# Kernel optimization log

Hardware: AMD Instinct MI355X
Metric: run time of the kernel (lower is better)

Reference implementation:

```python
import jax, jax.numpy as jnp
import numpy as np

N_NODES = 50000
N_EDGES = 800000
D_IN = 128
D_OUT = 128


def setup_inputs() -> dict:
    key = jax.random.key(0)
    k1, k2, k3, k4, k5, k6 = jax.random.split(key, 6)
    stdv = 1.0 / np.sqrt(D_OUT)
    x = jax.random.normal(k1, (N_NODES, D_IN), dtype=jnp.float32)
    weight = jax.random.uniform(k2, (D_IN, D_OUT), dtype=jnp.float32, minval=-stdv, maxval=stdv)
    bias = jax.random.uniform(k3, (D_OUT,), dtype=jnp.float32, minval=-stdv, maxval=stdv)
    edge_weight = jax.random.uniform(k4, (N_EDGES,), dtype=jnp.float32)
    edge_row = jax.random.randint(k5, (N_EDGES,), 0, N_NODES, dtype=jnp.int64)
    edge_col = jax.random.randint(k6, (N_EDGES,), 0, N_NODES, dtype=jnp.int64)
    return {"x": x, "weight": weight, "bias": bias,
            "edge_weight": edge_weight, "edge_row": edge_row, "edge_col": edge_col}


def reference(x, weight, bias, edge_weight, edge_row, edge_col):
    # support = input @ W   -> [N, D_OUT]
    support = x @ weight
    # spmm(adj, support): out[i] = sum over edges (i<-j) of a_ij * support[j]
    gathered = support[edge_col] * edge_weight[:, None]  # [E, D_OUT]
    out = jax.ops.segment_sum(gathered, edge_row, num_segments=N_NODES)
    return out + bias
```

## Files before the change

kernel.cpp:

```cpp
#include <hip/hip_runtime.h>
#include <hip/hip_bf16.h>

#define NN 50000
#define NE 800000
#define D 128

#define RPB 50
#define NB 1000
#define NBP 1024
#define CAP 1024
#define TILE 4096
#define NBIN 196
#define AROWS 64
#define TSTR 136

#define CASTB 1563
#define PACKB 4

#define XH_OFF   0
#define WF_OFF   3200000
#define CUR_OFF  3208192
#define REC_OFF  3209216

typedef short bf16x8 __attribute__((ext_vector_type(8)));
typedef float f32x4 __attribute__((ext_vector_type(4)));

__device__ inline unsigned short f2bf_u(float f) {
    __hip_bfloat16 h = __float2bfloat16(f);
    return __builtin_bit_cast(unsigned short, h);
}
__device__ inline unsigned pack2(float a, float b) {
    return (unsigned)f2bf_u(a) | ((unsigned)f2bf_u(b) << 16);
}
__device__ inline void acc8(float* acc, uint4 v, float w) {
    unsigned dw[4] = {v.x, v.y, v.z, v.w};
    #pragma unroll
    for (int i = 0; i < 4; ++i) {
        float lo = __int_as_float((int)(dw[i] << 16));
        float hi = __int_as_float((int)(dw[i] & 0xffff0000u));
        acc[2 * i]     += w * lo;
        acc[2 * i + 1] += w * hi;
    }
}

__global__ __launch_bounds__(512) void cast_bin_kernel(
    const float* __restrict__ x, const float* __restrict__ W,
    const int* __restrict__ erow, const int* __restrict__ ecol,
    const float* __restrict__ ew,
    unsigned* __restrict__ x_h4, unsigned short* __restrict__ Wf,
    int* __restrict__ cursor, int2* __restrict__ recs)
{
    __shared__ int  lhist[NBP];
    __shared__ int  lexcl[NBP];
    __shared__ int  lbase[NBP];
    __shared__ int  lpair[512];
    __shared__ int2 stag[TILE];

    int b = blockIdx.x;
    int t = threadIdx.x;

    if (b < CASTB) {
        int idx = b * 512 + t;
        if (idx < 800000) {
            const float4* x4 = (const float4*)x;
            float4 v0 = x4[idx * 2];
            float4 v1 = x4[idx * 2 + 1];
            uint4 o;
            o.x = pack2(v0.x, v0.y);
            o.y = pack2(v0.z, v0.w);
            o.z = pack2(v1.x, v1.y);
            o.w = pack2(v1.z, v1.w);
            ((uint4*)x_h4)[idx] = o;
        }
        return;
    }
    if (b < CASTB + PACKB) {
        int flat = (b - CASTB) * 512 + t;
        int lane = flat & 63;
        int c    = (flat >> 6) & 3;
        int nt   = flat >> 8;
        int col  = nt * 16 + (lane & 15);
        int kb   = c * 32 + (lane >> 4) * 8;
        unsigned d[4];
        #pragma unroll
        for (int jj = 0; jj < 4; ++jj) {
            float a  = W[(kb + 2 * jj) * D + col];
            float bb = W[(kb + 2 * jj + 1) * D + col];
            d[jj] = pack2(a, bb);
        }
        uint4 o; o.x = d[0]; o.y = d[1]; o.z = d[2]; o.w = d[3];
        ((uint4*)Wf)[flat] = o;
        return;
    }

    int base = (b - CASTB - PACKB) * TILE;
    int cnt = NE - base; if (cnt > TILE) cnt = TILE;

    lhist[t] = 0;
    lhist[t + 512] = 0;
    __syncthreads();

    int4 r[2], c[2]; float4 w[2]; bool val[2];
    #pragma unroll
    for (int g = 0; g < 2; ++g) {
        int i4 = (base >> 2) + t + g * 512;
        val[g] = (i4 * 4) < NE && (i4 * 4) < (base + TILE);
        if (val[g]) {
            r[g] = ((const int4*)erow)[i4];
            c[g] = ((const int4*)ecol)[i4];
            w[g] = ((const float4*)ew)[i4];
        }
    }
    #pragma unroll
    for (int g = 0; g < 2; ++g) {
        if (val[g]) {
            atomicAdd(&lhist[(unsigned)r[g].x / RPB], 1);
            atomicAdd(&lhist[(unsigned)r[g].y / RPB], 1);
            atomicAdd(&lhist[(unsigned)r[g].z / RPB], 1);
            atomicAdd(&lhist[(unsigned)r[g].w / RPB], 1);
        }
    }
    __syncthreads();

    int a0 = lhist[2 * t], a1 = lhist[2 * t + 1];
    lpair[t] = a0 + a1;
    __syncthreads();
    for (int off = 1; off < 512; off <<= 1) {
        int v = (t >= off) ? lpair[t - off] : 0;
        __syncthreads();
        lpair[t] += v;
        __syncthreads();
    }
    int exclp = lpair[t] - (a0 + a1);
    lexcl[2 * t]     = exclp;
    lexcl[2 * t + 1] = exclp + a0;
    lbase[2 * t]     = a0 ? atomicAdd(&cursor[2 * t], a0) : 0;
    lbase[2 * t + 1] = a1 ? atomicAdd(&cursor[2 * t + 1], a1) : 0;
    lhist[2 * t]     = exclp;
    lhist[2 * t + 1] = exclp + a0;
    __syncthreads();

    #pragma unroll
    for (int g = 0; g < 2; ++g) {
        if (val[g]) {
            int rr[4] = {r[g].x, r[g].y, r[g].z, r[g].w};
            int cc[4] = {c[g].x, c[g].y, c[g].z, c[g].w};
            float wwv[4] = {w[g].x, w[g].y, w[g].z, w[g].w};
            #pragma unroll
            for (int j = 0; j < 4; ++j) {
                int bk = (unsigned)rr[j] / RPB;
                int rank = atomicAdd(&lhist[bk], 1);
                int2 rec;
                rec.x = (rr[j] << 16) | cc[j];
                rec.y = __float_as_int(wwv[j]);
                stag[rank] = rec;
            }
        }
    }
    __syncthreads();

    #pragma unroll
    for (int k = 0; k < 8; ++k) {
        int i = t + k * 512;
        if (i < cnt) {
            int2 rec = stag[i];
            int bk = (((unsigned)rec.x) >> 16) / RPB;
            int pos = lbase[bk] + (i - lexcl[bk]);
            if (pos < CAP)
                recs[(size_t)bk * CAP + pos] = rec;
        }
    }
}

__global__ __launch_bounds__(512) void gat_gemm_kernel(
    const unsigned short* __restrict__ x_h, const int2* __restrict__ recs,
    const int* __restrict__ cursor, const unsigned short* __restrict__ Wf,
    const float* __restrict__ bias, float* __restrict__ out)
{
    __shared__ int2 srec[CAP];
    __shared__ __align__(16) unsigned short tile[AROWS * TSTR];
    __shared__ int rowstart[RPB + 1];
    __shared__ int rowcur[64];
    __shared__ int stmp[64];

    int t = threadIdx.x;
    int b = blockIdx.x;
    int cnt = cursor[b];
    if (cnt > CAP) cnt = CAP;
    int rb = b * RPB;
    const int2* my = recs + (size_t)b * CAP;

    if (t < 64) rowcur[t] = 0;
    __syncthreads();

    int2 r0, r1;
    bool v0 = t < cnt, v1 = t + 512 < cnt;
    if (v0) r0 = my[t];
    if (v1) r1 = my[t + 512];

    if (v0) atomicAdd(&rowcur[(((unsigned)r0.x) >> 16) - rb], 1);
    if (v1) atomicAdd(&rowcur[(((unsigned)r1.x) >> 16) - rb], 1);
    __syncthreads();

    int myc = 0;
    if (t < 64) { myc = rowcur[t]; stmp[t] = myc; }
    __syncthreads();
    for (int off = 1; off < 64; off <<= 1) {
        int v = 0;
        if (t < 64 && t >= off) v = stmp[t - off];
        __syncthreads();
        if (t < 64) stmp[t] += v;
        __syncthreads();
    }
    if (t < 64) { int ex = stmp[t] - myc; if (t <= RPB) rowstart[t] = ex; rowcur[t] = ex; }
    if (t == 0) rowstart[RPB] = cnt;
    __syncthreads();

    if (v0) srec[atomicAdd(&rowcur[(((unsigned)r0.x) >> 16) - rb], 1)] = r0;
    if (v1) srec[atomicAdd(&rowcur[(((unsigned)r1.x) >> 16) - rb], 1)] = r1;
    __syncthreads();

    int q = t & 15;
    int grp = t >> 4;
    const uint4* xv = (const uint4*)x_h;
    #pragma unroll
    for (int it = 0; it < 2; ++it) {
        int rl = it * 32 + grp;
        if (rl < RPB) {
            int p = rowstart[rl], p1 = rowstart[rl + 1];
            float acc[8] = {};
            for (; p + 4 <= p1; p += 4) {
                int2 e0 = srec[p];
                int2 e1 = srec[p + 1];
                int2 e2 = srec[p + 2];
                int2 e3 = srec[p + 3];
                uint4 w0 = xv[(size_t)(e0.x & 0xffff) * 16 + q];
                uint4 w1 = xv[(size_t)(e1.x & 0xffff) * 16 + q];
                uint4 w2 = xv[(size_t)(e2.x & 0xffff) * 16 + q];
                uint4 w3 = xv[(size_t)(e3.x & 0xffff) * 16 + q];
                acc8(acc, w0, __int_as_float(e0.y));
                acc8(acc, w1, __int_as_float(e1.y));
                acc8(acc, w2, __int_as_float(e2.y));
                acc8(acc, w3, __int_as_float(e3.y));
            }
            for (; p < p1; ++p) {
                int2 e = srec[p];
                uint4 w = xv[(size_t)(e.x & 0xffff) * 16 + q];
                acc8(acc, w, __int_as_float(e.y));
            }
            uint4 o;
            o.x = pack2(acc[0], acc[1]);
            o.y = pack2(acc[2], acc[3]);
            o.z = pack2(acc[4], acc[5]);
            o.w = pack2(acc[6], acc[7]);
            *(uint4*)&tile[rl * TSTR + q * 8] = o;
        }
    }
    __syncthreads();

    int wave = t >> 6, lane = t & 63;
    int m = lane & 15, quad = lane >> 4;
    const bf16x8* bp = (const bf16x8*)Wf;
    bf16x8 bfr[4];
    #pragma unroll
    for (int c = 0; c < 4; ++c) bfr[c] = bp[(wave * 4 + c) * 64 + lane];
    float bcol = bias[wave * 16 + m];

    #pragma unroll
    for (int mt = 0; mt < 4; ++mt) {
        f32x4 acc = {0.f, 0.f, 0.f, 0.f};
        #pragma unroll
        for (int c = 0; c < 4; ++c) {
            bf16x8 afr = *(const bf16x8*)&tile[(mt * 16 + m) * TSTR + c * 32 + quad * 8];
            acc = __builtin_amdgcn_mfma_f32_16x16x32_bf16(afr, bfr[c], acc, 0, 0, 0);
        }
        #pragma unroll
        for (int r = 0; r < 4; ++r) {
            int lr = mt * 16 + quad * 4 + r;
            int grow = rb + lr;
            if (lr < RPB && grow < NN)
                out[(size_t)grow * D + wave * 16 + m] = acc[r] + bcol;
        }
    }
}

extern "C" void kernel_launch(void* const* d_in, const int* in_sizes, int n_in,
                              void* d_out, int out_size, void* d_ws, size_t ws_size,
                              hipStream_t stream) {
    const float* x    = (const float*)d_in[0];
    const float* W    = (const float*)d_in[1];
    const float* bias = (const float*)d_in[2];
    const float* ew   = (const float*)d_in[3];
    const int*   erow = (const int*)d_in[4];
    const int*   ecol = (const int*)d_in[5];
    float* out = (float*)d_out;

    unsigned* ws_u = (unsigned*)d_ws;
    unsigned*        x_h4   = ws_u + XH_OFF;
    unsigned short*  x_h    = (unsigned short*)x_h4;
    unsigned short*  Wf     = (unsigned short*)(ws_u + WF_OFF);
    int*             cursor = (int*)(ws_u + CUR_OFF);
    int2*            recs   = (int2*)(ws_u + REC_OFF);

    hipMemsetAsync(cursor, 0, NBP * sizeof(int), stream);
    cast_bin_kernel<<<CASTB + PACKB + NBIN, 512, 0, stream>>>(
        x, W, erow, ecol, ew, x_h4, Wf, cursor, recs);
    gat_gemm_kernel<<<NB, 512, 0, stream>>>(x_h, recs, cursor, Wf, bias, out);
}
```

Measured before the change: 129.7 us.

## Use power-of-two row bins, direct global scatter, and wave-shuffle scan

After: 142.6 us. 10.0% more time.

```diff
diff --git a/kernel.cpp b/kernel.cpp
--- a/kernel.cpp
+++ b/kernel.cpp
@@ -5,22 +5,20 @@
 #define NE 800000
 #define D 128
 
-#define RPB 50
-#define NB 1000
-#define NBP 1024
-#define CAP 1024
-#define TILE 4096
-#define NBIN 196
-#define AROWS 64
+#define RPB 32
+#define NB 1563
+#define NBP2 2048
+#define CAP 768
+#define TILE 2048
+#define NBIN 391
+#define CASTB 782
+#define PACKB 4
 #define TSTR 136
-
-#define CASTB 1563
-#define PACKB 4
 
 #define XH_OFF   0
 #define WF_OFF   3200000
 #define CUR_OFF  3208192
-#define REC_OFF  3209216
+#define REC_OFF  3210240
 
 typedef short bf16x8 __attribute__((ext_vector_type(8)));
 typedef float f32x4 __attribute__((ext_vector_type(4)));
@@ -50,19 +48,85 @@
     unsigned* __restrict__ x_h4, unsigned short* __restrict__ Wf,
     int* __restrict__ cursor, int2* __restrict__ recs)
 {
-    __shared__ int  lhist[NBP];
-    __shared__ int  lexcl[NBP];
-    __shared__ int  lbase[NBP];
-    __shared__ int  lpair[512];
-    __shared__ int2 stag[TILE];
+    __shared__ int lhist[NBP2];
 
     int b = blockIdx.x;
     int t = threadIdx.x;
 
-    if (b < CASTB) {
-        int idx = b * 512 + t;
+    if (b < NBIN) {
+        #pragma unroll
+        for (int k = 0; k < 4; ++k) lhist[t + k * 512] = 0;
+        __syncthreads();
+
+        int base = b * TILE;
+        int i4 = (base >> 2) + t;
+        bool val = (i4 * 4) < NE;
+        int4 r, c; float4 w;
+        if (val) {
+            r = ((const int4*)erow)[i4];
+            c = ((const int4*)ecol)[i4];
+            w = ((const float4*)ew)[i4];
+        }
+        if (val) {
+            atomicAdd(&lhist[(unsigned)r.x >> 5], 1);
+            atomicAdd(&lhist[(unsigned)r.y >> 5], 1);
+            atomicAdd(&lhist[(unsigned)r.z >> 5], 1);
+            atomicAdd(&lhist[(unsigned)r.w >> 5], 1);
+        }
+        __syncthreads();
+
+        #pragma unroll
+        for (int k = 0; k < 4; ++k) {
+            int bin = t + k * 512;
+            int n = lhist[bin];
+            if (n > 0) lhist[bin] = atomicAdd(&cursor[bin], n);
+        }
+        __syncthreads();
+
+        if (val) {
+            int rr[4] = {r.x, r.y, r.z, r.w};
+            int cc[4] = {c.x, c.y, c.z, c.w};
+            float wwv[4] = {w.x, w.y, w.z, w.w};
+            #pragma unroll
+            for (int j = 0; j < 4; ++j) {
+                int bk = (unsigned)rr[j] >> 5;
+                int pos = atomicAdd(&lhist[bk], 1);
+                if (pos < CAP) {
+                    int2 rec;
+                    rec.x = (rr[j] << 16) | cc[j];
+                    rec.y = __float_as_int(wwv[j]);
+                    recs[(size_t)bk * CAP + pos] = rec;
+                }
+            }
+        }
+        return;
+    }
+
+    if (b < NBIN + PACKB) {
+        int flat = (b - NBIN) * 512 + t;
+        int lane = flat & 63;
+        int c    = (flat >> 6) & 3;
+        int nt   = flat >> 8;
+        int col  = nt * 16 + (lane & 15);
+        int kb   = c * 32 + (lane >> 4) * 8;
+        unsigned d[4];
+        #pragma unroll
+        for (int jj = 0; jj < 4; ++jj) {
+            float a  = W[(kb + 2 * jj) * D + col];
+            float bb = W[(kb + 2 * jj + 1) * D + col];
+            d[jj] = pack2(a, bb);
+        }
+        uint4 o; o.x = d[0]; o.y = d[1]; o.z = d[2]; o.w = d[3];
+        ((uint4*)Wf)[flat] = o;
+        return;
+    }
+
+    int base = (b - NBIN - PACKB) * 1024 + t;
+    const float4* x4 = (const float4*)x;
+    #pragma unroll
+    for (int g = 0; g < 2; ++g) {
+        int idx = base + g * 512;
         if (idx < 800000) {
-            const float4* x4 = (const float4*)x;
             float4 v0 = x4[idx * 2];
             float4 v1 = x4[idx * 2 + 1];
             uint4 o;
@@ -72,103 +136,6 @@
             o.w = pack2(v1.z, v1.w);
             ((uint4*)x_h4)[idx] = o;
         }
-        return;
-    }
-    if (b < CASTB + PACKB) {
-        int flat = (b - CASTB) * 512 + t;
-        int lane = flat & 63;
-        int c    = (flat >> 6) & 3;
-        int nt   = flat >> 8;
-        int col  = nt * 16 + (lane & 15);
-        int kb   = c * 32 + (lane >> 4) * 8;
-        unsigned d[4];
-        #pragma unroll
-        for (int jj = 0; jj < 4; ++jj) {
-            float a  = W[(kb + 2 * jj) * D + col];
-            float bb = W[(kb + 2 * jj + 1) * D + col];
-            d[jj] = pack2(a, bb);
-        }
-        uint4 o; o.x = d[0]; o.y = d[1]; o.z = d[2]; o.w = d[3];
-        ((uint4*)Wf)[flat] = o;
-        return;
-    }
-
-    int base = (b - CASTB - PACKB) * TILE;
-    int cnt = NE - base; if (cnt > TILE) cnt = TILE;
-
-    lhist[t] = 0;
-    lhist[t + 512] = 0;
-    __syncthreads();
-
-    int4 r[2], c[2]; float4 w[2]; bool val[2];
-    #pragma unroll
-    for (int g = 0; g < 2; ++g) {
-        int i4 = (base >> 2) + t + g * 512;
-        val[g] = (i4 * 4) < NE && (i4 * 4) < (base + TILE);
-        if (val[g]) {
-            r[g] = ((const int4*)erow)[i4];
-            c[g] = ((const int4*)ecol)[i4];
-            w[g] = ((const float4*)ew)[i4];
-        }
-    }
-    #pragma unroll
-    for (int g = 0; g < 2; ++g) {
-        if (val[g]) {
-            atomicAdd(&lhist[(unsigned)r[g].x / RPB], 1);
-            atomicAdd(&lhist[(unsigned)r[g].y / RPB], 1);
-            atomicAdd(&lhist[(unsigned)r[g].z / RPB], 1);
-            atomicAdd(&lhist[(unsigned)r[g].w / RPB], 1);
-        }
-    }
-    __syncthreads();
-
-    int a0 = lhist[2 * t], a1 = lhist[2 * t + 1];
-    lpair[t] = a0 + a1;
-    __syncthreads();
-    for (int off = 1; off < 512; off <<= 1) {
-        int v = (t >= off) ? lpair[t - off] : 0;
-        __syncthreads();
-        lpair[t] += v;
-        __syncthreads();
-    }
-    int exclp = lpair[t] - (a0 + a1);
-    lexcl[2 * t]     = exclp;
-    lexcl[2 * t + 1] = exclp + a0;
-    lbase[2 * t]     = a0 ? atomicAdd(&cursor[2 * t], a0) : 0;
-    lbase[2 * t + 1] = a1 ? atomicAdd(&cursor[2 * t + 1], a1) : 0;
-    lhist[2 * t]     = exclp;
-    lhist[2 * t + 1] = exclp + a0;
-    __syncthreads();
-
-    #pragma unroll
-    for (int g = 0; g < 2; ++g) {
-        if (val[g]) {
-            int rr[4] = {r[g].x, r[g].y, r[g].z, r[g].w};
-            int cc[4] = {c[g].x, c[g].y, c[g].z, c[g].w};
-            float wwv[4] = {w[g].x, w[g].y, w[g].z, w[g].w};
-            #pragma unroll
-            for (int j = 0; j < 4; ++j) {
-                int bk = (unsigned)rr[j] / RPB;
-                int rank = atomicAdd(&lhist[bk], 1);
-                int2 rec;
-                rec.x = (rr[j] << 16) | cc[j];
-                rec.y = __float_as_int(wwv[j]);
-                stag[rank] = rec;
-            }
-        }
-    }
-    __syncthreads();
-
-    #pragma unroll
-    for (int k = 0; k < 8; ++k) {
-        int i = t + k * 512;
-        if (i < cnt) {
-            int2 rec = stag[i];
-            int bk = (((unsigned)rec.x) >> 16) / RPB;
-            int pos = lbase[bk] + (i - lexcl[bk]);
-            if (pos < CAP)
-                recs[(size_t)bk * CAP + pos] = rec;
-        }
     }
 }
 
@@ -178,10 +145,9 @@
     const float* __restrict__ bias, float* __restrict__ out)
 {
     __shared__ int2 srec[CAP];
-    __shared__ __align__(16) unsigned short tile[AROWS * TSTR];
+    __shared__ __align__(16) unsigned short tile[RPB * TSTR];
     __shared__ int rowstart[RPB + 1];
-    __shared__ int rowcur[64];
-    __shared__ int stmp[64];
+    __shared__ int rowcur[RPB];
 
     int t = threadIdx.x;
     int b = blockIdx.x;
@@ -190,7 +156,7 @@
     int rb = b * RPB;
     const int2* my = recs + (size_t)b * CAP;
 
-    if (t < 64) rowcur[t] = 0;
+    if (t < RPB) rowcur[t] = 0;
     __syncthreads();
 
     int2 r0, r1;
@@ -198,63 +164,59 @@
     if (v0) r0 = my[t];
     if (v1) r1 = my[t + 512];
 
-    if (v0) atomicAdd(&rowcur[(((unsigned)r0.x) >> 16) - rb], 1);
-    if (v1) atomicAdd(&rowcur[(((unsigned)r1.x) >> 16) - rb], 1);
-    __syncthreads();
-
-    int myc = 0;
-    if (t < 64) { myc = rowcur[t]; stmp[t] = myc; }
-    __syncthreads();
-    for (int off = 1; off < 64; off <<= 1) {
-        int v = 0;
-        if (t < 64 && t >= off) v = stmp[t - off];
-        __syncthreads();
-        if (t < 64) stmp[t] += v;
-        __syncthreads();
-    }
-    if (t < 64) { int ex = stmp[t] - myc; if (t <= RPB) rowstart[t] = ex; rowcur[t] = ex; }
+    if (v0) atomicAdd(&rowcur[(((unsigned)r0.x) >> 16) & (RPB - 1)], 1);
+    if (v1) atomicAdd(&rowcur[(((unsigned)r1.x) >> 16) & (RPB - 1)], 1);
+    __syncthreads();
+
+    if (t < RPB) {
+        int myc = rowcur[t];
+        int s = myc;
+        #pragma unroll
+        for (int off = 1; off < RPB; off <<= 1) {
+            int v = __shfl_up(s, off);
+            if (t >= off) s += v;
+        }
+        rowstart[t] = s - myc;
+        rowcur[t]   = s - myc;
+    }
     if (t == 0) rowstart[RPB] = cnt;
     __syncthreads();
 
-    if (v0) srec[atomicAdd(&rowcur[(((unsigned)r0.x) >> 16) - rb], 1)] = r0;
-    if (v1) srec[atomicAdd(&rowcur[(((unsigned)r1.x) >> 16) - rb], 1)] = r1;
-    __syncthreads();
-
-    int q = t & 15;
-    int grp = t >> 4;
-    const uint4* xv = (const uint4*)x_h;
-    #pragma unroll
-    for (int it = 0; it < 2; ++it) {
-        int rl = it * 32 + grp;
-        if (rl < RPB) {
-            int p = rowstart[rl], p1 = rowstart[rl + 1];
-            float acc[8] = {};
-            for (; p + 4 <= p1; p += 4) {
-                int2 e0 = srec[p];
-                int2 e1 = srec[p + 1];
-                int2 e2 = srec[p + 2];
-                int2 e3 = srec[p + 3];
-                uint4 w0 = xv[(size_t)(e0.x & 0xffff) * 16 + q];
-                uint4 w1 = xv[(size_t)(e1.x & 0xffff) * 16 + q];
-                uint4 w2 = xv[(size_t)(e2.x & 0xffff) * 16 + q];
-                uint4 w3 = xv[(size_t)(e3.x & 0xffff) * 16 + q];
-                acc8(acc, w0, __int_as_float(e0.y));
-                acc8(acc, w1, __int_as_float(e1.y));
-                acc8(acc, w2, __int_as_float(e2.y));
-                acc8(acc, w3, __int_as_float(e3.y));
-            }
-            for (; p < p1; ++p) {
-                int2 e = srec[p];
-                uint4 w = xv[(size_t)(e.x & 0xffff) * 16 + q];
-                acc8(acc, w, __int_as_float(e.y));
-            }
-            uint4 o;
-            o.x = pack2(acc[0], acc[1]);
-            o.y = pack2(acc[2], acc[3]);
-            o.z = pack2(acc[4], acc[5]);
-            o.w = pack2(acc[6], acc[7]);
-            *(uint4*)&tile[rl * TSTR + q * 8] = o;
-        }
+    if (v0) srec[atomicAdd(&rowcur[(((unsigned)r0.x) >> 16) & (RPB - 1)], 1)] = r0;
+    if (v1) srec[atomicAdd(&rowcur[(((unsigned)r1.x) >> 16) & (RPB - 1)], 1)] = r1;
+    __syncthreads();
+
+    {
+        int q = t & 15;
+        int rl = t >> 4;
+        const uint4* xv = (const uint4*)x_h;
+        int p = rowstart[rl], p1 = rowstart[rl + 1];
+        float acc[8] = {};
+        for (; p + 4 <= p1; p += 4) {
+            int2 e0 = srec[p];
+            int2 e1 = srec[p + 1];
+            int2 e2 = srec[p + 2];
+            int2 e3 = srec[p + 3];
+            uint4 w0 = xv[(size_t)(e0.x & 0xffff) * 16 + q];
+            uint4 w1 = xv[(size_t)(e1.x & 0xffff) * 16 + q];
+            uint4 w2 = xv[(size_t)(e2.x & 0xffff) * 16 + q];
+            uint4 w3 = xv[(size_t)(e3.x & 0xffff) * 16 + q];
+            acc8(acc, w0, __int_as_float(e0.y));
+            acc8(acc, w1, __int_as_float(e1.y));
+            acc8(acc, w2, __int_as_float(e2.y));
+            acc8(acc, w3, __int_as_float(e3.y));
+        }
+        for (; p < p1; ++p) {
+            int2 e = srec[p];
+            uint4 w = xv[(size_t)(e.x & 0xffff) * 16 + q];
+            acc8(acc, w, __int_as_float(e.y));
+        }
+        uint4 o;
+        o.x = pack2(acc[0], acc[1]);
+        o.y = pack2(acc[2], acc[3]);
+        o.z = pack2(acc[4], acc[5]);
+        o.w = pack2(acc[6], acc[7]);
+        *(uint4*)&tile[rl * TSTR + q * 8] = o;
     }
     __syncthreads();
 
@@ -267,7 +229,7 @@
     float bcol = bias[wave * 16 + m];
 
     #pragma unroll
-    for (int mt = 0; mt < 4; ++mt) {
+    for (int mt = 0; mt < 2; ++mt) {
         f32x4 acc = {0.f, 0.f, 0.f, 0.f};
         #pragma unroll
         for (int c = 0; c < 4; ++c) {
@@ -278,7 +240,7 @@
         for (int r = 0; r < 4; ++r) {
             int lr = mt * 16 + quad * 4 + r;
             int grow = rb + lr;
-            if (lr < RPB && grow < NN)
+            if (grow < NN)
                 out[(size_t)grow * D + wave * 16 + m] = acc[r] + bcol;
         }
     }
@@ -302,8 +264,8 @@
     int*             cursor = (int*)(ws_u + CUR_OFF);
     int2*            recs   = (int2*)(ws_u + REC_OFF);
 
-    hipMemsetAsync(cursor, 0, NBP * sizeof(int), stream);
-    cast_bin_kernel<<<CASTB + PACKB + NBIN, 512, 0, stream>>>(
+    hipMemsetAsync(cursor, 0, NBP2 * sizeof(int), stream);
+    cast_bin_kernel<<<NBIN + PACKB + CASTB, 512, 0, stream>>>(
         x, W, erow, ecol, ew, x_h4, Wf, cursor, recs);
     gat_gemm_kernel<<<NB, 512, 0, stream>>>(x_h, recs, cursor, Wf, bias, out);
 }
```

## Use 64 rows per bucket with shift indexing and wave-shuffle scan

Applied to the files above, without the earlier changes.

Result: slower. 132.5 us (+2.2%).

```diff
diff --git a/kernel.cpp b/kernel.cpp
--- a/kernel.cpp
+++ b/kernel.cpp
@@ -5,10 +5,10 @@
 #define NE 800000
 #define D 128
 
-#define RPB 50
-#define NB 1000
+#define RPB 64
+#define NB 782
 #define NBP 1024
-#define CAP 1024
+#define CAP 1408
 #define TILE 4096
 #define NBIN 196
 #define AROWS 64
@@ -104,7 +104,7 @@
     #pragma unroll
     for (int g = 0; g < 2; ++g) {
         int i4 = (base >> 2) + t + g * 512;
-        val[g] = (i4 * 4) < NE && (i4 * 4) < (base + TILE);
+        val[g] = (i4 * 4) < NE;
         if (val[g]) {
             r[g] = ((const int4*)erow)[i4];
             c[g] = ((const int4*)ecol)[i4];
@@ -114,10 +114,10 @@
     #pragma unroll
     for (int g = 0; g < 2; ++g) {
         if (val[g]) {
-            atomicAdd(&lhist[(unsigned)r[g].x / RPB], 1);
-            atomicAdd(&lhist[(unsigned)r[g].y / RPB], 1);
-            atomicAdd(&lhist[(unsigned)r[g].z / RPB], 1);
-            atomicAdd(&lhist[(unsigned)r[g].w / RPB], 1);
+            atomicAdd(&lhist[(unsigned)r[g].x >> 6], 1);
+            atomicAdd(&lhist[(unsigned)r[g].y >> 6], 1);
+            atomicAdd(&lhist[(unsigned)r[g].z >> 6], 1);
+            atomicAdd(&lhist[(unsigned)r[g].w >> 6], 1);
         }
     }
     __syncthreads();
@@ -148,7 +148,7 @@
             float wwv[4] = {w[g].x, w[g].y, w[g].z, w[g].w};
             #pragma unroll
             for (int j = 0; j < 4; ++j) {
-                int bk = (unsigned)rr[j] / RPB;
+                int bk = (unsigned)rr[j] >> 6;
                 int rank = atomicAdd(&lhist[bk], 1);
                 int2 rec;
                 rec.x = (rr[j] << 16) | cc[j];
@@ -164,7 +164,7 @@
         int i = t + k * 512;
         if (i < cnt) {
             int2 rec = stag[i];
-            int bk = (((unsigned)rec.x) >> 16) / RPB;
+            int bk = (((unsigned)rec.x) >> 16) >> 6;
             int pos = lbase[bk] + (i - lexcl[bk]);
             if (pos < CAP)
                 recs[(size_t)bk * CAP + pos] = rec;
@@ -180,8 +180,7 @@
     __shared__ int2 srec[CAP];
     __shared__ __align__(16) unsigned short tile[AROWS * TSTR];
     __shared__ int rowstart[RPB + 1];
-    __shared__ int rowcur[64];
-    __shared__ int stmp[64];
+    __shared__ int rowcur[RPB];
 
     int t = threadIdx.x;
     int b = blockIdx.x;
@@ -190,34 +189,37 @@
     int rb = b * RPB;
     const int2* my = recs + (size_t)b * CAP;
 
-    if (t < 64) rowcur[t] = 0;
-    __syncthreads();
-
-    int2 r0, r1;
-    bool v0 = t < cnt, v1 = t + 512 < cnt;
+    if (t < RPB) rowcur[t] = 0;
+    __syncthreads();
+
+    int2 r0, r1, r2;
+    bool v0 = t < cnt, v1 = t + 512 < cnt, v2 = t + 1024 < cnt;
     if (v0) r0 = my[t];
     if (v1) r1 = my[t + 512];
-
-    if (v0) atomicAdd(&rowcur[(((unsigned)r0.x) >> 16) - rb], 1);
-    if (v1) atomicAdd(&rowcur[(((unsigned)r1.x) >> 16) - rb], 1);
-    __syncthreads();
-
-    int myc = 0;
-    if (t < 64) { myc = rowcur[t]; stmp[t] = myc; }
-    __syncthreads();
-    for (int off = 1; off < 64; off <<= 1) {
-        int v = 0;
-        if (t < 64 && t >= off) v = stmp[t - off];
-        __syncthreads();
-        if (t < 64) stmp[t] += v;
-        __syncthreads();
-    }
-    if (t < 64) { int ex = stmp[t] - myc; if (t <= RPB) rowstart[t] = ex; rowcur[t] = ex; }
+    if (v2) r2 = my[t + 1024];
+
+    if (v0) atomicAdd(&rowcur[(((unsigned)r0.x) >> 16) & (RPB - 1)], 1);
+    if (v1) atomicAdd(&rowcur[(((unsigned)r1.x) >> 16) & (RPB - 1)], 1);
+    if (v2) atomicAdd(&rowcur[(((unsigned)r2.x) >> 16) & (RPB - 1)], 1);
+    __syncthreads();
+
+    if (t < RPB) {
+        int myc = rowcur[t];
+        int s = myc;
+        #pragma unroll
+        for (int off = 1; off < RPB; off <<= 1) {
+            int v = __shfl_up(s, off);
+            if (t >= off) s += v;
+        }
+        rowstart[t] = s - myc;
+        rowcur[t]   = s - myc;
+    }
     if (t == 0) rowstart[RPB] = cnt;
     __syncthreads();
 
-    if (v0) srec[atomicAdd(&rowcur[(((unsigned)r0.x) >> 16) - rb], 1)] = r0;
-    if (v1) srec[atomicAdd(&rowcur[(((unsigned)r1.x) >> 16) - rb], 1)] = r1;
+    if (v0) srec[atomicAdd(&rowcur[(((unsigned)r0.x) >> 16) & (RPB - 1)], 1)] = r0;
+    if (v1) srec[atomicAdd(&rowcur[(((unsigned)r1.x) >> 16) & (RPB - 1)], 1)] = r1;
+    if (v2) srec[atomicAdd(&rowcur[(((unsigned)r2.x) >> 16) & (RPB - 1)], 1)] = r2;
     __syncthreads();
 
     int q = t & 15;
@@ -226,35 +228,33 @@
     #pragma unroll
     for (int it = 0; it < 2; ++it) {
         int rl = it * 32 + grp;
-        if (rl < RPB) {
-            int p = rowstart[rl], p1 = rowstart[rl + 1];
-            float acc[8] = {};
-            for (; p + 4 <= p1; p += 4) {
-                int2 e0 = srec[p];
-                int2 e1 = srec[p + 1];
-                int2 e2 = srec[p + 2];
-                int2 e3 = srec[p + 3];
-                uint4 w0 = xv[(size_t)(e0.x & 0xffff) * 16 + q];
-                uint4 w1 = xv[(size_t)(e1.x & 0xffff) * 16 + q];
-                uint4 w2 = xv[(size_t)(e2.x & 0xffff) * 16 + q];
-                uint4 w3 = xv[(size_t)(e3.x & 0xffff) * 16 + q];
-                acc8(acc, w0, __int_as_float(e0.y));
-                acc8(acc, w1, __int_as_float(e1.y));
-                acc8(acc, w2, __int_as_float(e2.y));
-                acc8(acc, w3, __int_as_float(e3.y));
-            }
-            for (; p < p1; ++p) {
-                int2 e = srec[p];
-                uint4 w = xv[(size_t)(e.x & 0xffff) * 16 + q];
-                acc8(acc, w, __int_as_float(e.y));
-            }
-            uint4 o;
-            o.x = pack2(acc[0], acc[1]);
-            o.y = pack2(acc[2], acc[3]);
-            o.z = pack2(acc[4], acc[5]);
-            o.w = pack2(acc[6], acc[7]);
-            *(uint4*)&tile[rl * TSTR + q * 8] = o;
-        }
+        int p = rowstart[rl], p1 = rowstart[rl + 1];
+        float acc[8] = {};
+        for (; p + 4 <= p1; p += 4) {
+            int2 e0 = srec[p];
+            int2 e1 = srec[p + 1];
+            int2 e2 = srec[p + 2];
+            int2 e3 = srec[p + 3];
+            uint4 w0 = xv[(size_t)(e0.x & 0xffff) * 16 + q];
+            uint4 w1 = xv[(size_t)(e1.x & 0xffff) * 16 + q];
+            uint4 w2 = xv[(size_t)(e2.x & 0xffff) * 16 + q];
+            uint4 w3 = xv[(size_t)(e3.x & 0xffff) * 16 + q];
+            acc8(acc, w0, __int_as_float(e0.y));
+            acc8(acc, w1, __int_as_float(e1.y));
+            acc8(acc, w2, __int_as_float(e2.y));
+            acc8(acc, w3, __int_as_float(e3.y));
+        }
+        for (; p < p1; ++p) {
+            int2 e = srec[p];
+            uint4 w = xv[(size_t)(e.x & 0xffff) * 16 + q];
+            acc8(acc, w, __int_as_float(e.y));
+        }
+        uint4 o;
+        o.x = pack2(acc[0], acc[1]);
+        o.y = pack2(acc[2], acc[3]);
+        o.z = pack2(acc[4], acc[5]);
+        o.w = pack2(acc[6], acc[7]);
+        *(uint4*)&tile[rl * TSTR + q * 8] = o;
     }
     __syncthreads();
 
@@ -278,7 +278,7 @@
         for (int r = 0; r < 4; ++r) {
             int lr = mt * 16 + quad * 4 + r;
             int grow = rb + lr;
-            if (lr < RPB && grow < NN)
+            if (grow < NN)
                 out[(size_t)grow * D + wave * 16 + m] = acc[r] + bcol;
         }
     }
```
